# Kernel optimization log

Hardware: AMD Instinct MI355X
Metric: run time of the kernel (lower is better)

The kernel has to match this reference:

```python
import jax, jax.numpy as jnp
import numpy as np

# Large finite negative used for masking inside the softmax chain. exp(NEG - m)
# underflows to exactly 0.0 in fp32, so valid positions match the torch -inf
# masking bit-for-bit; masked output positions are set to -inf at the end.
NEG = jnp.float32(-1e30)

B, L, F = 8192, 128, 64


def setup_inputs() -> dict:
    key = jax.random.key(0)
    k1, k2, k3 = jax.random.split(key, 3)
    return {
        "choice_set_features": jax.random.normal(k1, (B, L, F), dtype=jnp.float32),
        "choice_set_lengths": jax.random.randint(k2, (B,), 1, L + 1),  # in [1, L]
        "thetas": jax.random.uniform(k3, (F, F), dtype=jnp.float32),   # torch.rand init
        "mixture_weights": jnp.ones((F,), dtype=jnp.float32),
    }


def reference(choice_set_features, choice_set_lengths, thetas, mixture_weights):
    b, l, f = choice_set_features.shape
    # utilities[b,l,g] = x[b,l,:] @ thetas[g,:]   (x @ thetas.T)
    util = jnp.einsum('blf,gf->blg', choice_set_features, thetas)
    pad = jnp.arange(l)[None, :] >= choice_set_lengths[:, None]  # [B, L] True = padded
    util = jnp.where(pad[..., None], NEG, util)
    # log_softmax over the choice-set dimension (dim 1), per mixture component
    log_probs = jax.nn.log_softmax(util, axis=1)
    # mixture over components (dim 2) with log-softmaxed mixture weights
    out = jax.nn.logsumexp(log_probs + jax.nn.log_softmax(mixture_weights), axis=2)
    # padded slots are exactly -inf in the torch reference
    return jnp.where(pad, -jnp.inf, out)
```

## Files before the change

### kernel.cpp

```cpp
#include <hip/hip_runtime.h>
#include <math.h>

#define NEGV  (-1e30f)
#define LOG2E 1.44269504088896340736f
#define LN2   0.69314718055994530942f

typedef __attribute__((ext_vector_type(8))) _Float16 half8;
typedef __attribute__((ext_vector_type(2))) __fp16   fp16x2;
typedef __attribute__((ext_vector_type(4))) float f32x4;

__device__ __forceinline__ float exp2_fast(float a) { return __builtin_amdgcn_exp2f(a); }
__device__ __forceinline__ float log2_fast(float a) { return __builtin_amdgcn_logf(a); }

__device__ __forceinline__ half8 cvt8(float4 a, float4 b) {
    union { half8 v; fp16x2 p[4]; } u;
    u.p[0] = __builtin_amdgcn_cvt_pkrtz(a.x, a.y);
    u.p[1] = __builtin_amdgcn_cvt_pkrtz(a.z, a.w);
    u.p[2] = __builtin_amdgcn_cvt_pkrtz(b.x, b.y);
    u.p[3] = __builtin_amdgcn_cvt_pkrtz(b.z, b.w);
    return u.v;
}

#define WS_FLOATS_NEEDED (64 + 8 * 64 * 4)

__global__ void prep_kernel(const float* __restrict__ theta,
                            const float* __restrict__ mw,
                            float* __restrict__ ws)
{
    const int lane = threadIdx.x;
    const int c15  = lane & 15;
    const int q    = lane >> 4;

    const float v = mw[lane];
    float m = v;
#pragma unroll
    for (int s = 32; s >= 1; s >>= 1) m = fmaxf(m, __shfl_xor(m, s, 64));
    float e = __expf(v - m);
#pragma unroll
    for (int s = 32; s >= 1; s >>= 1) e += __shfl_xor(e, s, 64);
    const float logZ = m + __logf(e);
    ws[lane] = (v - logZ) * LOG2E;

#pragma unroll
    for (int gt = 0; gt < 4; ++gt) {
        const float* tr = theta + (size_t)((gt << 4) + c15) * 64 + (q << 3);
#pragma unroll
        for (int kt = 0; kt < 2; ++kt) {
            float4 a = *(const float4*)(tr + kt * 32);
            float4 c = *(const float4*)(tr + kt * 32 + 4);
            a.x *= LOG2E; a.y *= LOG2E; a.z *= LOG2E; a.w *= LOG2E;
            c.x *= LOG2E; c.y *= LOG2E; c.z *= LOG2E; c.w *= LOG2E;
            const half8 h = cvt8(a, c);
            const int s = (gt << 1) + kt;
            *(half8*)&ws[64 + ((size_t)(s * 64 + lane)) * 4] = h;
        }
    }
}

template<bool USE_WS>
__global__ __launch_bounds__(256, 4) void mixed_logit_kernel(
    const float* __restrict__ x,
    const int*   __restrict__ lens,
    const float* __restrict__ theta,
    const float* __restrict__ mw,
    const float* __restrict__ ws,
    float* __restrict__ out)
{
    __shared__ __align__(16) unsigned char lds_p[64 * 272];
    __shared__ __align__(16) float lds_c[64];

    const int tid  = threadIdx.x;
    const int lane = tid & 63;
    const int w    = tid >> 6;
    const int c15  = lane & 15;
    const int q    = lane >> 4;
    const int b    = blockIdx.x;
    const int len  = lens[b];

    half8 th[4][2];
    float logZ_fb = 0.f;
    if constexpr (USE_WS) {
#pragma unroll
        for (int gt = 0; gt < 4; ++gt)
#pragma unroll
            for (int kt = 0; kt < 2; ++kt)
                th[gt][kt] = *(const half8*)&ws[64 + ((size_t)((((gt << 1) + kt) * 64) + lane)) * 4];
    } else {
#pragma unroll
        for (int gt = 0; gt < 4; ++gt) {
            const float* tr = theta + (size_t)((gt << 4) + c15) * 64 + (q << 3);
#pragma unroll
            for (int kt = 0; kt < 2; ++kt) {
                float4 a = *(const float4*)(tr + kt * 32);
                float4 c = *(const float4*)(tr + kt * 32 + 4);
                a.x *= LOG2E; a.y *= LOG2E; a.z *= LOG2E; a.w *= LOG2E;
                c.x *= LOG2E; c.y *= LOG2E; c.z *= LOG2E; c.w *= LOG2E;
                th[gt][kt] = cvt8(a, c);
            }
        }
        const float mwl = mw[lane];
        float mmax = mwl;
#pragma unroll
        for (int s = 32; s >= 1; s >>= 1) mmax = fmaxf(mmax, __shfl_xor(mmax, s, 64));
        float me = __expf(mwl - mmax);
#pragma unroll
        for (int s = 32; s >= 1; s >>= 1) me += __shfl_xor(me, s, 64);
        logZ_fb = mmax + __logf(me);
    }

    half8 xf[2][2];
    {
        const float* xb = x + (size_t)b * 8192;
#pragma unroll
        for (int lt_loc = 0; lt_loc < 2; ++lt_loc) {
            const int row = (w << 5) + (lt_loc << 4) + c15;
#pragma unroll
            for (int kt = 0; kt < 2; ++kt) {
                const float* p = xb + (size_t)row * 64 + kt * 32 + (q << 3);
                xf[lt_loc][kt] = cvt8(*(const float4*)p, *(const float4*)(p + 4));
            }
        }
    }

    f32x4 acc[4][2];
#pragma unroll
    for (int gt = 0; gt < 4; ++gt)
#pragma unroll
        for (int lt = 0; lt < 2; ++lt) acc[gt][lt] = (f32x4){0.f, 0.f, 0.f, 0.f};

#pragma unroll
    for (int gt = 0; gt < 4; ++gt)
#pragma unroll
        for (int lt = 0; lt < 2; ++lt)
#pragma unroll
            for (int kt = 0; kt < 2; ++kt)
                acc[gt][lt] = __builtin_amdgcn_mfma_f32_16x16x32_f16(th[gt][kt], xf[lt][kt], acc[gt][lt], 0, 0, 0);

    {
        const int l0 = (w << 5) + c15;
        const bool v0 = l0 < len;
        const bool v1 = (l0 + 16) < len;
#pragma unroll
        for (int gt = 0; gt < 4; ++gt)
#pragma unroll
            for (int i = 0; i < 4; ++i) {
                acc[gt][0][i] = v0 ? acc[gt][0][i] : NEGV;
                acc[gt][1][i] = v1 ? acc[gt][1][i] : NEGV;
            }
    }

    {
        unsigned char* base = lds_p + ((w << 4) + c15) * 272 + (q << 4);
#pragma unroll
        for (int gt = 0; gt < 4; ++gt) {
            f32x4 p1;
#pragma unroll
            for (int i = 0; i < 4; ++i)
                p1[i] = exp2_fast(acc[gt][0][i]) + exp2_fast(acc[gt][1][i]);
            *(f32x4*)(base + (gt << 6)) = p1;
        }
    }
    __syncthreads();

    {
        const int gg = (w << 4) + (lane >> 2);
        const int r4 = lane & 3;
        float s = 0.f;
#pragma unroll
        for (int k = 0; k < 16; ++k) {
            const int rr = (r4 << 4) + ((k + (r4 << 2)) & 15);
            s += *(const float*)(lds_p + rr * 272 + (gg << 2));
        }
        s += __shfl_xor(s, 1, 64);
        s += __shfl_xor(s, 2, 64);
        if (r4 == 0) {
            float wgv;
            if constexpr (USE_WS) wgv = ws[gg];
            else                  wgv = (mw[gg] - logZ_fb) * LOG2E;
            lds_c[gg] = wgv - log2_fast(s);
        }
    }
    __syncthreads();

    {
        f32x4 c4[4];
#pragma unroll
        for (int gt = 0; gt < 4; ++gt)
            c4[gt] = *(const f32x4*)((const unsigned char*)lds_c + (gt << 6) + (q << 4));

#pragma unroll
        for (int lt = 0; lt < 2; ++lt) {
            float s2 = 0.f;
#pragma unroll
            for (int gt = 0; gt < 4; ++gt)
#pragma unroll
                for (int i = 0; i < 4; ++i)
                    s2 += exp2_fast(acc[gt][lt][i] + c4[gt][i]);
            s2 += __shfl_xor(s2, 16, 64);
            s2 += __shfl_xor(s2, 32, 64);
            if (q == 0) {
                const int l = (w << 5) + (lt << 4) + c15;
                out[(size_t)b * 128 + l] = (l < len) ? LN2 * log2_fast(s2) : NEGV;
            }
        }
    }
}

extern "C" void kernel_launch(void* const* d_in, const int* in_sizes, int n_in,
                              void* d_out, int out_size, void* d_ws, size_t ws_size,
                              hipStream_t stream) {
    const float* x     = (const float*)d_in[0];
    const int*   lens  = (const int*)d_in[1];
    const float* theta = (const float*)d_in[2];
    const float* mw    = (const float*)d_in[3];
    float* out = (float*)d_out;
    const int B = in_sizes[1];

    if (ws_size >= (size_t)WS_FLOATS_NEEDED * sizeof(float)) {
        float* ws = (float*)d_ws;
        prep_kernel<<<1, 64, 0, stream>>>(theta, mw, ws);
        mixed_logit_kernel<true><<<B, 256, 0, stream>>>(x, lens, theta, mw, ws, out);
    } else {
        mixed_logit_kernel<false><<<B, 256, 0, stream>>>(x, lens, theta, mw, nullptr, out);
    }
}
```

Baseline: 53.13 us.

## Use one wavefront per batch row with LDS-staged fp16 x and register softmax

```diff
diff --git a/kernel.cpp b/kernel.cpp
--- a/kernel.cpp
+++ b/kernel.cpp
@@ -58,7 +58,7 @@
 }
 
 template<bool USE_WS>
-__global__ __launch_bounds__(256, 4) void mixed_logit_kernel(
+__global__ __launch_bounds__(64, 2) void mixed_logit_kernel(
     const float* __restrict__ x,
     const int*   __restrict__ lens,
     const float* __restrict__ theta,
@@ -66,25 +66,40 @@
     const float* __restrict__ ws,
     float* __restrict__ out)
 {
-    __shared__ __align__(16) unsigned char lds_p[64 * 272];
-    __shared__ __align__(16) float lds_c[64];
-
-    const int tid  = threadIdx.x;
-    const int lane = tid & 63;
-    const int w    = tid >> 6;
+    __shared__ __align__(16) unsigned char xbuf[128 * 144];
+
+    const int lane = threadIdx.x;
     const int c15  = lane & 15;
     const int q    = lane >> 4;
     const int b    = blockIdx.x;
     const int len  = lens[b];
 
+    {
+        const float4* xp = (const float4*)(x + (size_t)b * 8192);
+#pragma unroll
+        for (int k = 0; k < 16; ++k) {
+            const int j2 = (k << 6) + lane;
+            const float4 a = xp[j2 * 2];
+            const float4 c = xp[j2 * 2 + 1];
+            const half8 h = cvt8(a, c);
+            *(half8*)(xbuf + (j2 >> 3) * 144 + (j2 & 7) * 16) = h;
+        }
+    }
+
     half8 th[4][2];
-    float logZ_fb = 0.f;
+    float wg[4][4];
     if constexpr (USE_WS) {
 #pragma unroll
         for (int gt = 0; gt < 4; ++gt)
 #pragma unroll
             for (int kt = 0; kt < 2; ++kt)
                 th[gt][kt] = *(const half8*)&ws[64 + ((size_t)((((gt << 1) + kt) * 64) + lane)) * 4];
+#pragma unroll
+        for (int gt = 0; gt < 4; ++gt) {
+            const f32x4 wv = *(const f32x4*)&ws[(gt << 4) + (q << 2)];
+#pragma unroll
+            for (int i = 0; i < 4; ++i) wg[gt][i] = wv[i];
+        }
     } else {
 #pragma unroll
         for (int gt = 0; gt < 4; ++gt) {
@@ -105,103 +120,74 @@
         float me = __expf(mwl - mmax);
 #pragma unroll
         for (int s = 32; s >= 1; s >>= 1) me += __shfl_xor(me, s, 64);
-        logZ_fb = mmax + __logf(me);
-    }
-
-    half8 xf[2][2];
-    {
-        const float* xb = x + (size_t)b * 8192;
-#pragma unroll
-        for (int lt_loc = 0; lt_loc < 2; ++lt_loc) {
-            const int row = (w << 5) + (lt_loc << 4) + c15;
-#pragma unroll
-            for (int kt = 0; kt < 2; ++kt) {
-                const float* p = xb + (size_t)row * 64 + kt * 32 + (q << 3);
-                xf[lt_loc][kt] = cvt8(*(const float4*)p, *(const float4*)(p + 4));
+        const float logZ = mmax + __logf(me);
+#pragma unroll
+        for (int gt = 0; gt < 4; ++gt)
+#pragma unroll
+            for (int i = 0; i < 4; ++i)
+                wg[gt][i] = (mw[(gt << 4) + (q << 2) + i] - logZ) * LOG2E;
+    }
+
+    f32x4 acc[4][8];
+#pragma unroll
+    for (int gt = 0; gt < 4; ++gt)
+#pragma unroll
+        for (int nt = 0; nt < 8; ++nt) acc[gt][nt] = (f32x4){0.f, 0.f, 0.f, 0.f};
+
+#pragma unroll
+    for (int nt = 0; nt < 8; ++nt) {
+        const unsigned char* rb = xbuf + ((nt << 4) + c15) * 144 + (q << 4);
+        const half8 x0 = *(const half8*)(rb);
+        const half8 x1 = *(const half8*)(rb + 64);
+#pragma unroll
+        for (int gt = 0; gt < 4; ++gt) {
+            acc[gt][nt] = __builtin_amdgcn_mfma_f32_16x16x32_f16(th[gt][0], x0, acc[gt][nt], 0, 0, 0);
+            acc[gt][nt] = __builtin_amdgcn_mfma_f32_16x16x32_f16(th[gt][1], x1, acc[gt][nt], 0, 0, 0);
+        }
+    }
+
+    bool vm[8];
+#pragma unroll
+    for (int nt = 0; nt < 8; ++nt) vm[nt] = ((nt << 4) + c15) < len;
+
+#pragma unroll
+    for (int gt = 0; gt < 4; ++gt)
+#pragma unroll
+        for (int nt = 0; nt < 8; ++nt)
+#pragma unroll
+            for (int i = 0; i < 4; ++i) {
+                const float pv = exp2_fast(acc[gt][nt][i]);
+                acc[gt][nt][i] = vm[nt] ? pv : 0.f;
             }
-        }
-    }
-
-    f32x4 acc[4][2];
+
+    float e4[4][4];
 #pragma unroll
     for (int gt = 0; gt < 4; ++gt)
 #pragma unroll
-        for (int lt = 0; lt < 2; ++lt) acc[gt][lt] = (f32x4){0.f, 0.f, 0.f, 0.f};
-
-#pragma unroll
-    for (int gt = 0; gt < 4; ++gt)
-#pragma unroll
-        for (int lt = 0; lt < 2; ++lt)
-#pragma unroll
-            for (int kt = 0; kt < 2; ++kt)
-                acc[gt][lt] = __builtin_amdgcn_mfma_f32_16x16x32_f16(th[gt][kt], xf[lt][kt], acc[gt][lt], 0, 0, 0);
-
-    {
-        const int l0 = (w << 5) + c15;
-        const bool v0 = l0 < len;
-        const bool v1 = (l0 + 16) < len;
-#pragma unroll
-        for (int gt = 0; gt < 4; ++gt)
-#pragma unroll
-            for (int i = 0; i < 4; ++i) {
-                acc[gt][0][i] = v0 ? acc[gt][0][i] : NEGV;
-                acc[gt][1][i] = v1 ? acc[gt][1][i] : NEGV;
-            }
-    }
-
-    {
-        unsigned char* base = lds_p + ((w << 4) + c15) * 272 + (q << 4);
-#pragma unroll
-        for (int gt = 0; gt < 4; ++gt) {
-            f32x4 p1;
-#pragma unroll
-            for (int i = 0; i < 4; ++i)
-                p1[i] = exp2_fast(acc[gt][0][i]) + exp2_fast(acc[gt][1][i]);
-            *(f32x4*)(base + (gt << 6)) = p1;
-        }
-    }
-    __syncthreads();
-
-    {
-        const int gg = (w << 4) + (lane >> 2);
-        const int r4 = lane & 3;
-        float s = 0.f;
-#pragma unroll
-        for (int k = 0; k < 16; ++k) {
-            const int rr = (r4 << 4) + ((k + (r4 << 2)) & 15);
-            s += *(const float*)(lds_p + rr * 272 + (gg << 2));
-        }
-        s += __shfl_xor(s, 1, 64);
-        s += __shfl_xor(s, 2, 64);
-        if (r4 == 0) {
-            float wgv;
-            if constexpr (USE_WS) wgv = ws[gg];
-            else                  wgv = (mw[gg] - logZ_fb) * LOG2E;
-            lds_c[gg] = wgv - log2_fast(s);
-        }
-    }
-    __syncthreads();
-
-    {
-        f32x4 c4[4];
-#pragma unroll
-        for (int gt = 0; gt < 4; ++gt)
-            c4[gt] = *(const f32x4*)((const unsigned char*)lds_c + (gt << 6) + (q << 4));
-
-#pragma unroll
-        for (int lt = 0; lt < 2; ++lt) {
-            float s2 = 0.f;
-#pragma unroll
-            for (int gt = 0; gt < 4; ++gt)
-#pragma unroll
-                for (int i = 0; i < 4; ++i)
-                    s2 += exp2_fast(acc[gt][lt][i] + c4[gt][i]);
-            s2 += __shfl_xor(s2, 16, 64);
-            s2 += __shfl_xor(s2, 32, 64);
-            if (q == 0) {
-                const int l = (w << 5) + (lt << 4) + c15;
-                out[(size_t)b * 128 + l] = (l < len) ? LN2 * log2_fast(s2) : NEGV;
-            }
+        for (int i = 0; i < 4; ++i) {
+            float e = 0.f;
+#pragma unroll
+            for (int nt = 0; nt < 8; ++nt) e += acc[gt][nt][i];
+#pragma unroll
+            for (int s = 1; s < 16; s <<= 1) e += __shfl_xor(e, s, 64);
+            e4[gt][i] = exp2_fast(wg[gt][i] - log2_fast(e));
+        }
+
+#pragma unroll
+    for (int nt = 0; nt < 8; ++nt) {
+        float s2 = 0.f;
+#pragma unroll
+        for (int gt = 0; gt < 4; ++gt) {
+            s2 = fmaf(acc[gt][nt][0], e4[gt][0], s2);
+            s2 = fmaf(acc[gt][nt][1], e4[gt][1], s2);
+            s2 = fmaf(acc[gt][nt][2], e4[gt][2], s2);
+            s2 = fmaf(acc[gt][nt][3], e4[gt][3], s2);
+        }
+        s2 += __shfl_xor(s2, 16, 64);
+        s2 += __shfl_xor(s2, 32, 64);
+        if (q == 0) {
+            const int l = (nt << 4) + c15;
+            out[(size_t)b * 128 + l] = (l < len) ? LN2 * log2_fast(s2) : NEGV;
         }
     }
 }
@@ -219,8 +205,8 @@
     if (ws_size >= (size_t)WS_FLOATS_NEEDED * sizeof(float)) {
         float* ws = (float*)d_ws;
         prep_kernel<<<1, 64, 0, stream>>>(theta, mw, ws);
-        mixed_logit_kernel<true><<<B, 256, 0, stream>>>(x, lens, theta, mw, ws, out);
+        mixed_logit_kernel<true><<<B, 64, 0, stream>>>(x, lens, theta, mw, ws, out);
     } else {
-        mixed_logit_kernel<false><<<B, 256, 0, stream>>>(x, lens, theta, mw, nullptr, out);
-    }
-}
+        mixed_logit_kernel<false><<<B, 64, 0, stream>>>(x, lens, theta, mw, nullptr, out);
+    }
+}
```

Measured after the change: 53.58 us. About the same (+0.9%).
